# Kernel tuning notes

Measured on AMD Instinct MI355X. Metric: run time of the kernel, lower is better.

## Reference

```python
import jax, jax.numpy as jnp
import numpy as np

NUM_EMBEDDINGS = 1024
EMBEDDING_DIM = 64
COMMITMENT_COST = 0.25
EPS_NORM = 1e-12  # torch F.normalize eps


def _l2_normalize(x):
    n = jnp.linalg.norm(x, axis=-1, keepdims=True)
    return x / jnp.maximum(n, EPS_NORM)


def setup_inputs() -> dict:
    key = jax.random.key(0)
    k1, k2 = jax.random.split(key)
    inputs = jax.random.normal(k1, (16, 4096, EMBEDDING_DIM), dtype=jnp.float32)
    weight = jax.random.normal(k2, (NUM_EMBEDDINGS, EMBEDDING_DIM), dtype=jnp.float32) * 0.02
    return {"inputs": inputs, "weight": weight}


def reference(inputs, weight):
    input_shape = inputs.shape
    x = _l2_normalize(inputs)                      # [B,S,D]
    flat = x.reshape(-1, EMBEDDING_DIM)            # [N,D]
    w = _l2_normalize(weight)                      # [K,D]

    distances = (jnp.sum(flat ** 2, axis=1, keepdims=True)
                 + jnp.sum(w ** 2, axis=1)
                 - 2.0 * flat @ w.T)               # [N,K]
    encoding_indices = jnp.argmin(distances, axis=1)  # [N]

    quantized = w[encoding_indices].reshape(input_shape)  # [B,S,D]

    e_latent_loss = jnp.mean((jax.lax.stop_gradient(quantized) - x) ** 2)
    q_latent_loss = jnp.mean((quantized - jax.lax.stop_gradient(x)) ** 2)
    loss = q_latent_loss + COMMITMENT_COST * e_latent_loss

    # straight-through estimator
    quantized_ste = x + jax.lax.stop_gradient(quantized - x)

    # perplexity (no-grad bookkeeping)
    n = encoding_indices.shape[0]
    counts = jnp.zeros((NUM_EMBEDDINGS,), jnp.float32).at[encoding_indices].add(1.0)
    avg_probs = counts / n
    perplexity = jnp.exp(-jnp.sum(avg_probs * jnp.log(avg_probs + 1e-10)))

    return loss, quantized_ste, perplexity, encoding_indices[:, None]
```

## Files before the change

### kernel.cpp

```cpp
#include <hip/hip_runtime.h>
#include <hip/hip_bf16.h>
#include <math.h>

#define NROWS   65536
#define DIM     64
#define KCODES  1024
#define NBLOCKS (NROWS / 128)

#define QGAP 1.25e-4f

typedef short short8 __attribute__((ext_vector_type(8)));
typedef float f32x4  __attribute__((ext_vector_type(4)));

#define OUT_Q_OFF    ((size_t)1)
#define OUT_PERP_OFF ((size_t)(1 + (size_t)NROWS * DIM))
#define OUT_IDX_OFF  ((size_t)(2 + (size_t)NROWS * DIM))

#define WS_COUNTS 0
#define WS_SSEC   4096
#define WS_DONE   4100
#define WS_WN     8192
#define WS_SK     (WS_WN + KCODES*DIM*4)
#define WS_WNH    (WS_SK + KCODES*4)
#define WS_WNL    (WS_WNH + KCODES*DIM*2)

__device__ __forceinline__ unsigned short bf16_rne(float f) {
  unsigned u = __float_as_uint(f);
  return (unsigned short)((u + 0x7FFFu + ((u >> 16) & 1u)) >> 16);
}
__device__ __forceinline__ float bf16f(unsigned short h) {
  return __uint_as_float(((unsigned)h) << 16);
}

__global__ void __launch_bounds__(64) normalize_w_kernel(
    const float* __restrict__ w, float* __restrict__ wn, float* __restrict__ sk,
    unsigned short* __restrict__ wnh, unsigned short* __restrict__ wnl,
    unsigned* __restrict__ counts, float* __restrict__ sse_accum,
    unsigned* __restrict__ done) {
  const int k = blockIdx.x;
  const int d = threadIdx.x;
  if (d == 0) {
    counts[k] = 0u;
    if (k == 0) { *sse_accum = 0.f; *done = 0u; }
  }
  float v = w[k * DIM + d];
  float ss = v * v;
  #pragma unroll
  for (int o = 32; o > 0; o >>= 1) ss += __shfl_xor(ss, o, 64);
  const float den = fmaxf(sqrtf(ss), 1e-12f);
  const float q = v / den;
  wn[k * DIM + d] = q;
  const unsigned short h = bf16_rne(q);
  wnh[k * DIM + d] = h;
  wnl[k * DIM + d] = bf16_rne(q - bf16f(h));
  float s2 = q * q;
  #pragma unroll
  for (int o = 32; o > 0; o >>= 1) s2 += __shfl_xor(s2, o, 64);
  if (d == 0) sk[k] = s2;
}

__global__ void __launch_bounds__(256) vq_mega_kernel(
    const float* __restrict__ x, const unsigned short* __restrict__ wnh,
    const unsigned short* __restrict__ wnl, const float* __restrict__ sk,
    const float* __restrict__ wn, float* __restrict__ out,
    unsigned* __restrict__ counts, float* __restrict__ sse_accum,
    unsigned* __restrict__ done) {
  __shared__ unsigned AB[9216];
  __shared__ float skb[2][64];
  __shared__ float c_arr[128];
  __shared__ float rowsse[128];
  __shared__ int   ib[128];
  __shared__ int   qlist[128];
  __shared__ int   qn_s;
  __shared__ int   islast;
  const int tid = threadIdx.x;
  const int lane = tid & 63, wave = tid >> 6;

  if (tid == 0) qn_s = 0;

  if (tid < 128) {
    const size_t row = (size_t)blockIdx.x * 128 + tid;
    const float4* xr = (const float4*)(x + row * DIM);
    float4 xv[16];
    float ss = 0.f;
    #pragma unroll
    for (int i = 0; i < 16; i++) {
      xv[i] = xr[i];
      ss += xv[i].x * xv[i].x + xv[i].y * xv[i].y + xv[i].z * xv[i].z + xv[i].w * xv[i].w;
    }
    const float inv = 1.0f / fmaxf(sqrtf(ss), 1e-12f);
    float c = 0.f;
    #pragma unroll
    for (int i = 0; i < 16; i++) {
      const float a0 = xv[i].x * inv, a1 = xv[i].y * inv;
      const float a2 = xv[i].z * inv, a3 = xv[i].w * inv;
      c += a0 * a0 + a1 * a1 + a2 * a2 + a3 * a3;
      const unsigned short h0 = bf16_rne(a0), h1 = bf16_rne(a1);
      const unsigned short h2 = bf16_rne(a2), h3 = bf16_rne(a3);
      const unsigned short l0 = bf16_rne(a0 - bf16f(h0)), l1 = bf16_rne(a1 - bf16f(h1));
      const unsigned short l2 = bf16_rne(a2 - bf16f(h2)), l3 = bf16_rne(a3 - bf16f(h3));
      AB[tid * 36 + 2 * i]            = (unsigned)h0 | ((unsigned)h1 << 16);
      AB[tid * 36 + 2 * i + 1]        = (unsigned)h2 | ((unsigned)h3 << 16);
      AB[4608 + tid * 36 + 2 * i]     = (unsigned)l0 | ((unsigned)l1 << 16);
      AB[4608 + tid * 36 + 2 * i + 1] = (unsigned)l2 | ((unsigned)l3 << 16);
    }
    c_arr[tid] = c;
  }
  __syncthreads();

  short8 ah[2][2], al[2][2];
  #pragma unroll
  for (int rt = 0; rt < 2; rt++)
    #pragma unroll
    for (int kk = 0; kk < 2; kk++) {
      const int r = wave * 32 + rt * 16 + (lane & 15);
      ah[rt][kk] = *(const short8*)&AB[r * 36 + kk * 16 + (lane >> 4) * 4];
      al[rt][kk] = *(const short8*)&AB[4608 + r * 36 + kk * 16 + (lane >> 4) * 4];
    }
  __syncthreads();

  float d1[8], d2[8];
  int   i1[8];
  #pragma unroll
  for (int s = 0; s < 8; s++) { d1[s] = INFINITY; d2[s] = INFINITY; i1[s] = 0x7FFFFFFF; }

  {
    const int code = tid >> 2, q = tid & 3;
    const float4* gh = (const float4*)(wnh + (size_t)code * DIM + q * 16);
    const float4* gl = (const float4*)(wnl + (size_t)code * DIM + q * 16);
    float4* dh = (float4*)&AB[code * 36 + q * 8];
    float4* dl = (float4*)&AB[2304 + code * 36 + q * 8];
    dh[0] = gh[0]; dh[1] = gh[1];
    dl[0] = gl[0]; dl[1] = gl[1];
    if (tid < 64) skb[0][tid] = sk[tid];
  }

  #pragma unroll 2
  for (int c = 0; c < 16; c++) {
    const int b = c & 1;
    __syncthreads();
    if (c < 15) {
      const int nb = b ^ 1;
      const int code = tid >> 2, q = tid & 3;
      const float4* gh = (const float4*)(wnh + (size_t)((c + 1) * 64 + code) * DIM + q * 16);
      const float4* gl = (const float4*)(wnl + (size_t)((c + 1) * 64 + code) * DIM + q * 16);
      float4* dh = (float4*)&AB[nb * 4608 + code * 36 + q * 8];
      float4* dl = (float4*)&AB[nb * 4608 + 2304 + code * 36 + q * 8];
      dh[0] = gh[0]; dh[1] = gh[1];
      dl[0] = gl[0]; dl[1] = gl[1];
      if (tid < 64) skb[nb][tid] = sk[(c + 1) * 64 + tid];
    }
    #pragma unroll
    for (int tt = 0; tt < 4; tt++) {
      const int cb = tt * 16 + (lane & 15);
      const float skv = skb[b][cb];
      const int codev = c * 64 + cb;
      const short8 bh0 = *(const short8*)&AB[b * 4608 + cb * 36 + 0 * 16 + (lane >> 4) * 4];
      const short8 bh1 = *(const short8*)&AB[b * 4608 + cb * 36 + 1 * 16 + (lane >> 4) * 4];
      const short8 bl0 = *(const short8*)&AB[b * 4608 + 2304 + cb * 36 + 0 * 16 + (lane >> 4) * 4];
      const short8 bl1 = *(const short8*)&AB[b * 4608 + 2304 + cb * 36 + 1 * 16 + (lane >> 4) * 4];
      #pragma unroll
      for (int rt = 0; rt < 2; rt++) {
        f32x4 acc = {0.f, 0.f, 0.f, 0.f};
        acc = __builtin_amdgcn_mfma_f32_16x16x32_bf16(ah[rt][0], bh0, acc, 0, 0, 0);
        acc = __builtin_amdgcn_mfma_f32_16x16x32_bf16(ah[rt][1], bh1, acc, 0, 0, 0);
        acc = __builtin_amdgcn_mfma_f32_16x16x32_bf16(al[rt][0], bh0, acc, 0, 0, 0);
        acc = __builtin_amdgcn_mfma_f32_16x16x32_bf16(al[rt][1], bh1, acc, 0, 0, 0);
        acc = __builtin_amdgcn_mfma_f32_16x16x32_bf16(ah[rt][0], bl0, acc, 0, 0, 0);
        acc = __builtin_amdgcn_mfma_f32_16x16x32_bf16(ah[rt][1], bl1, acc, 0, 0, 0);
        #pragma unroll
        for (int i = 0; i < 4; i++) {
          const float dist = fmaf(-2.0f, acc[i], skv);
          const int s = rt * 4 + i;
          d2[s] = __builtin_amdgcn_fmed3f(d1[s], d2[s], dist);
          const bool take = dist < d1[s];
          d1[s] = take ? dist : d1[s];
          i1[s] = take ? codev : i1[s];
        }
      }
    }
  }

  #pragma unroll
  for (int s = 0; s < 8; s++) {
    float a1 = d1[s], a2 = d2[s];
    int   ai = i1[s];
    #pragma unroll
    for (int m = 1; m < 16; m <<= 1) {
      const float p1 = __shfl_xor(a1, m, 64);
      const float p2 = __shfl_xor(a2, m, 64);
      const int   pi = __shfl_xor(ai, m, 64);
      const float mx = fmaxf(a1, p1);
      a2 = fminf(fminf(a2, p2), mx);
      const bool take = (p1 < a1) || (p1 == a1 && pi < ai);
      a1 = take ? p1 : a1;
      ai = take ? pi : ai;
    }
    if ((lane & 15) == 0) {
      const int row_local = wave * 32 + (s >> 2) * 16 + (lane >> 4) * 4 + (s & 3);
      ib[row_local] = ai;
      rowsse[row_local] = a1 + c_arr[row_local];
      if (a2 - a1 < QGAP) qlist[atomicAdd(&qn_s, 1)] = row_local;
    }
  }
  __syncthreads();

  const int qn = qn_s;
  for (int qi = wave; qi < qn; qi += 4) {
    const int rl = qlist[qi];
    const size_t row = (size_t)blockIdx.x * 128 + rl;
    const float4* xr = (const float4*)(x + row * DIM);
    float4 xv[16];
    float ss = 0.f;
    #pragma unroll
    for (int i = 0; i < 16; i++) {
      xv[i] = xr[i];
      ss += xv[i].x * xv[i].x + xv[i].y * xv[i].y + xv[i].z * xv[i].z + xv[i].w * xv[i].w;
    }
    const float den = fmaxf(sqrtf(ss), 1e-12f);
    #pragma unroll
    for (int i = 0; i < 16; i++) { xv[i].x /= den; xv[i].y /= den; xv[i].z /= den; xv[i].w /= den; }
    float cc = 0.f;
    #pragma unroll
    for (int i = 0; i < 16; i++)
      cc += xv[i].x * xv[i].x + xv[i].y * xv[i].y + xv[i].z * xv[i].z + xv[i].w * xv[i].w;

    float best = INFINITY;
    int bidx = 0x7FFFFFFF;
    for (int j = 0; j < 16; j++) {
      const int k = j * 64 + lane;
      const float4* wr = (const float4*)(wn + (size_t)k * DIM);
      float e0 = 0.f, e1 = 0.f, e2 = 0.f, e3 = 0.f;
      #pragma unroll
      for (int i = 0; i < 16; i++) {
        const float4 wv = wr[i];
        e0 = fmaf(xv[i].x, wv.x, e0);
        e1 = fmaf(xv[i].y, wv.y, e1);
        e2 = fmaf(xv[i].z, wv.z, e2);
        e3 = fmaf(xv[i].w, wv.w, e3);
      }
      const float dot = (e0 + e1) + (e2 + e3);
      const float dist = (cc + sk[k]) - 2.0f * dot;
      if (dist < best) { best = dist; bidx = k; }
    }
    #pragma unroll
    for (int m = 1; m < 64; m <<= 1) {
      const float pb = __shfl_xor(best, m, 64);
      const int pi = __shfl_xor(bidx, m, 64);
      if (pb < best || (pb == best && pi < bidx)) { best = pb; bidx = pi; }
    }
    if (lane == 0) { ib[rl] = bidx; rowsse[rl] = best; }
  }
  __syncthreads();

  if (tid < 128) {
    const size_t row = (size_t)blockIdx.x * 128 + tid;
    const int idx = ib[tid];
    out[OUT_IDX_OFF + row] = (float)idx;
    atomicAdd(&counts[idx], 1u);
  }

  const size_t obase = OUT_Q_OFF + (size_t)blockIdx.x * (128 * DIM);
  #pragma unroll 4
  for (int j = 0; j < 32; j++) {
    const int e = j * 256 + tid;
    out[obase + e] = wn[(size_t)ib[e >> 6] * DIM + (e & 63)];
  }

  __syncthreads();
  for (int s = 64; s > 0; s >>= 1) {
    if (tid < s && tid + s < 128) rowsse[tid] += rowsse[tid + s];
    __syncthreads();
  }
  if (tid == 0) atomicAdd(sse_accum, rowsse[0]);

  if (tid == 0) {
    __threadfence();
    islast = (atomicAdd(done, 1u) == NBLOCKS - 1) ? 1 : 0;
  }
  __syncthreads();
  if (islast) {
    __threadfence();
    float h = 0.f;
    #pragma unroll
    for (int i = 0; i < 4; i++) {
      const float cv = (float)counts[tid * 4 + i];
      const float avg = cv * (1.0f / (float)NROWS);
      h += avg * logf(avg + 1e-10f);
    }
    #pragma unroll
    for (int o = 32; o > 0; o >>= 1) h += __shfl_xor(h, o, 64);
    __shared__ float hred[4];
    if (lane == 0) hred[wave] = h;
    __syncthreads();
    if (tid == 0) {
      const float H = -(hred[0] + hred[1] + hred[2] + hred[3]);
      const float mse = *sse_accum * (1.0f / (float)((size_t)NROWS * DIM));
      out[0] = mse + 0.25f * mse;
      out[OUT_PERP_OFF] = expf(H);
    }
  }
}

extern "C" void kernel_launch(void* const* d_in, const int* in_sizes, int n_in,
                              void* d_out, int out_size, void* d_ws, size_t ws_size,
                              hipStream_t stream) {
  const float* x = (const float*)d_in[0];
  const float* w = (const float*)d_in[1];
  float* out = (float*)d_out;

  char* ws = (char*)d_ws;
  unsigned* counts    = (unsigned*)(ws + WS_COUNTS);
  float* sse_accum    = (float*)(ws + WS_SSEC);
  unsigned* done      = (unsigned*)(ws + WS_DONE);
  float* wn           = (float*)(ws + WS_WN);
  float* sk           = (float*)(ws + WS_SK);
  unsigned short* wnh = (unsigned short*)(ws + WS_WNH);
  unsigned short* wnl = (unsigned short*)(ws + WS_WNL);

  normalize_w_kernel<<<KCODES, 64, 0, stream>>>(w, wn, sk, wnh, wnl,
                                                counts, sse_accum, done);
  vq_mega_kernel<<<NBLOCKS, 256, 0, stream>>>(
      x, wnh, wnl, sk, wn, out, counts, sse_accum, done);
}
```

Baseline: 144.8 us.

## Halve rows per block and track top-3 to cheapen near-tie rechecks

Rows per block drop from 128 to 64, which doubles the grid, and each wave now handles one 16-row tile instead of two. Input normalisation is split across four threads per row, with shuffle reductions. The argmin now tracks the best three distances and the top two indices. Rows whose top-2 gap is small but whose third candidate is clear get a cheap exact fp32 recheck of only two codes, one thread per row. Only rows with a three-way near tie fall back to the full 1024-code scan. The aim is better occupancy and less fallback work, at the cost of restaging the codebook twice as often (more L2 traffic) and extra comparison logic per distance.

```diff
diff --git a/kernel.cpp b/kernel.cpp
--- a/kernel.cpp
+++ b/kernel.cpp
@@ -5,7 +5,8 @@
 #define NROWS   65536
 #define DIM     64
 #define KCODES  1024
-#define NBLOCKS (NROWS / 128)
+#define RPB     64
+#define NBLOCKS (NROWS / RPB)
 
 #define QGAP 1.25e-4f
 
@@ -67,31 +68,35 @@
     unsigned* __restrict__ done) {
   __shared__ unsigned AB[9216];
   __shared__ float skb[2][64];
-  __shared__ float c_arr[128];
-  __shared__ float rowsse[128];
-  __shared__ int   ib[128];
-  __shared__ int   qlist[128];
-  __shared__ int   qn_s;
+  __shared__ float c_arr[RPB];
+  __shared__ float rowsse[RPB];
+  __shared__ int   ib[RPB];
+  __shared__ int   qlist[RPB];
+  __shared__ int   flist[RPB];
+  __shared__ int   qn_s, fn_s;
   __shared__ int   islast;
   const int tid = threadIdx.x;
   const int lane = tid & 63, wave = tid >> 6;
 
-  if (tid == 0) qn_s = 0;
-
-  if (tid < 128) {
-    const size_t row = (size_t)blockIdx.x * 128 + tid;
-    const float4* xr = (const float4*)(x + row * DIM);
-    float4 xv[16];
+  if (tid == 0) { qn_s = 0; fn_s = 0; }
+
+  {
+    const int row_l = tid >> 2;
+    const int qr = tid & 3;
+    const size_t row = (size_t)blockIdx.x * RPB + row_l;
+    const float4* xr = (const float4*)(x + row * DIM) + qr * 4;
+    float4 xv[4];
     float ss = 0.f;
     #pragma unroll
-    for (int i = 0; i < 16; i++) {
+    for (int i = 0; i < 4; i++) {
       xv[i] = xr[i];
       ss += xv[i].x * xv[i].x + xv[i].y * xv[i].y + xv[i].z * xv[i].z + xv[i].w * xv[i].w;
     }
+    ss += __shfl_xor(ss, 1, 64); ss += __shfl_xor(ss, 2, 64);
     const float inv = 1.0f / fmaxf(sqrtf(ss), 1e-12f);
     float c = 0.f;
     #pragma unroll
-    for (int i = 0; i < 16; i++) {
+    for (int i = 0; i < 4; i++) {
       const float a0 = xv[i].x * inv, a1 = xv[i].y * inv;
       const float a2 = xv[i].z * inv, a3 = xv[i].w * inv;
       c += a0 * a0 + a1 * a1 + a2 * a2 + a3 * a3;
@@ -99,30 +104,32 @@
       const unsigned short h2 = bf16_rne(a2), h3 = bf16_rne(a3);
       const unsigned short l0 = bf16_rne(a0 - bf16f(h0)), l1 = bf16_rne(a1 - bf16f(h1));
       const unsigned short l2 = bf16_rne(a2 - bf16f(h2)), l3 = bf16_rne(a3 - bf16f(h3));
-      AB[tid * 36 + 2 * i]            = (unsigned)h0 | ((unsigned)h1 << 16);
-      AB[tid * 36 + 2 * i + 1]        = (unsigned)h2 | ((unsigned)h3 << 16);
-      AB[4608 + tid * 36 + 2 * i]     = (unsigned)l0 | ((unsigned)l1 << 16);
-      AB[4608 + tid * 36 + 2 * i + 1] = (unsigned)l2 | ((unsigned)l3 << 16);
-    }
-    c_arr[tid] = c;
-  }
-  __syncthreads();
-
-  short8 ah[2][2], al[2][2];
-  #pragma unroll
-  for (int rt = 0; rt < 2; rt++)
-    #pragma unroll
-    for (int kk = 0; kk < 2; kk++) {
-      const int r = wave * 32 + rt * 16 + (lane & 15);
-      ah[rt][kk] = *(const short8*)&AB[r * 36 + kk * 16 + (lane >> 4) * 4];
-      al[rt][kk] = *(const short8*)&AB[4608 + r * 36 + kk * 16 + (lane >> 4) * 4];
-    }
-  __syncthreads();
-
-  float d1[8], d2[8];
-  int   i1[8];
-  #pragma unroll
-  for (int s = 0; s < 8; s++) { d1[s] = INFINITY; d2[s] = INFINITY; i1[s] = 0x7FFFFFFF; }
+      AB[row_l * 36 + qr * 8 + 2 * i]            = (unsigned)h0 | ((unsigned)h1 << 16);
+      AB[row_l * 36 + qr * 8 + 2 * i + 1]        = (unsigned)h2 | ((unsigned)h3 << 16);
+      AB[2304 + row_l * 36 + qr * 8 + 2 * i]     = (unsigned)l0 | ((unsigned)l1 << 16);
+      AB[2304 + row_l * 36 + qr * 8 + 2 * i + 1] = (unsigned)l2 | ((unsigned)l3 << 16);
+    }
+    c += __shfl_xor(c, 1, 64); c += __shfl_xor(c, 2, 64);
+    if (qr == 0) c_arr[row_l] = c;
+  }
+  __syncthreads();
+
+  short8 ah[2], al[2];
+  #pragma unroll
+  for (int kk = 0; kk < 2; kk++) {
+    const int r = wave * 16 + (lane & 15);
+    ah[kk] = *(const short8*)&AB[r * 36 + kk * 16 + (lane >> 4) * 4];
+    al[kk] = *(const short8*)&AB[2304 + r * 36 + kk * 16 + (lane >> 4) * 4];
+  }
+  __syncthreads();
+
+  float d1[4], d2[4], d3[4];
+  int   i1[4], i2[4];
+  #pragma unroll
+  for (int s = 0; s < 4; s++) {
+    d1[s] = INFINITY; d2[s] = INFINITY; d3[s] = INFINITY;
+    i1[s] = 0x7FFFFFFF; i2[s] = 0x7FFFFFFF;
+  }
 
   {
     const int code = tid >> 2, q = tid & 3;
@@ -159,56 +166,107 @@
       const short8 bh1 = *(const short8*)&AB[b * 4608 + cb * 36 + 1 * 16 + (lane >> 4) * 4];
       const short8 bl0 = *(const short8*)&AB[b * 4608 + 2304 + cb * 36 + 0 * 16 + (lane >> 4) * 4];
       const short8 bl1 = *(const short8*)&AB[b * 4608 + 2304 + cb * 36 + 1 * 16 + (lane >> 4) * 4];
+      f32x4 acc = {0.f, 0.f, 0.f, 0.f};
+      acc = __builtin_amdgcn_mfma_f32_16x16x32_bf16(ah[0], bh0, acc, 0, 0, 0);
+      acc = __builtin_amdgcn_mfma_f32_16x16x32_bf16(ah[1], bh1, acc, 0, 0, 0);
+      acc = __builtin_amdgcn_mfma_f32_16x16x32_bf16(al[0], bh0, acc, 0, 0, 0);
+      acc = __builtin_amdgcn_mfma_f32_16x16x32_bf16(al[1], bh1, acc, 0, 0, 0);
+      acc = __builtin_amdgcn_mfma_f32_16x16x32_bf16(ah[0], bl0, acc, 0, 0, 0);
+      acc = __builtin_amdgcn_mfma_f32_16x16x32_bf16(ah[1], bl1, acc, 0, 0, 0);
       #pragma unroll
-      for (int rt = 0; rt < 2; rt++) {
-        f32x4 acc = {0.f, 0.f, 0.f, 0.f};
-        acc = __builtin_amdgcn_mfma_f32_16x16x32_bf16(ah[rt][0], bh0, acc, 0, 0, 0);
-        acc = __builtin_amdgcn_mfma_f32_16x16x32_bf16(ah[rt][1], bh1, acc, 0, 0, 0);
-        acc = __builtin_amdgcn_mfma_f32_16x16x32_bf16(al[rt][0], bh0, acc, 0, 0, 0);
-        acc = __builtin_amdgcn_mfma_f32_16x16x32_bf16(al[rt][1], bh1, acc, 0, 0, 0);
-        acc = __builtin_amdgcn_mfma_f32_16x16x32_bf16(ah[rt][0], bl0, acc, 0, 0, 0);
-        acc = __builtin_amdgcn_mfma_f32_16x16x32_bf16(ah[rt][1], bl1, acc, 0, 0, 0);
-        #pragma unroll
-        for (int i = 0; i < 4; i++) {
-          const float dist = fmaf(-2.0f, acc[i], skv);
-          const int s = rt * 4 + i;
-          d2[s] = __builtin_amdgcn_fmed3f(d1[s], d2[s], dist);
-          const bool take = dist < d1[s];
-          d1[s] = take ? dist : d1[s];
-          i1[s] = take ? codev : i1[s];
-        }
+      for (int i = 0; i < 4; i++) {
+        const float dist = fmaf(-2.0f, acc[i], skv);
+        const int s = i;
+        d3[s] = __builtin_amdgcn_fmed3f(d2[s], d3[s], fmaxf(d1[s], dist));
+        const bool lt2 = dist < d2[s];
+        i2[s] = lt2 ? codev : i2[s];
+        d2[s] = __builtin_amdgcn_fmed3f(d1[s], d2[s], dist);
+        const bool lt1 = dist < d1[s];
+        i2[s] = lt1 ? i1[s] : i2[s];
+        i1[s] = lt1 ? codev : i1[s];
+        d1[s] = lt1 ? dist : d1[s];
       }
     }
   }
 
   #pragma unroll
-  for (int s = 0; s < 8; s++) {
-    float a1 = d1[s], a2 = d2[s];
-    int   ai = i1[s];
+  for (int s = 0; s < 4; s++) {
+    float a1 = d1[s], a2 = d2[s], a3 = d3[s];
+    int   ai = i1[s], ai2 = i2[s];
     #pragma unroll
     for (int m = 1; m < 16; m <<= 1) {
       const float p1 = __shfl_xor(a1, m, 64);
       const float p2 = __shfl_xor(a2, m, 64);
+      const float p3 = __shfl_xor(a3, m, 64);
       const int   pi = __shfl_xor(ai, m, 64);
-      const float mx = fmaxf(a1, p1);
-      a2 = fminf(fminf(a2, p2), mx);
+      const int   pi2 = __shfl_xor(ai2, m, 64);
       const bool take = (p1 < a1) || (p1 == a1 && pi < ai);
-      a1 = take ? p1 : a1;
-      ai = take ? pi : ai;
+      const float lo1 = take ? p1 : a1, lo2 = take ? p2 : a2, lo3 = take ? p3 : a3;
+      const float hi1 = take ? a1 : p1, hi2 = take ? a2 : p2;
+      const int   loi = take ? pi : ai, loi2 = take ? pi2 : ai2;
+      const int   hii = take ? ai : pi;
+      const bool c2 = hi1 < lo2;
+      a1 = lo1; ai = loi;
+      a2 = c2 ? hi1 : lo2; ai2 = c2 ? hii : loi2;
+      a3 = c2 ? fminf(lo2, hi2) : fminf(lo3, hi1);
     }
     if ((lane & 15) == 0) {
-      const int row_local = wave * 32 + (s >> 2) * 16 + (lane >> 4) * 4 + (s & 3);
+      const int row_local = wave * 16 + (lane >> 4) * 4 + s;
       ib[row_local] = ai;
       rowsse[row_local] = a1 + c_arr[row_local];
-      if (a2 - a1 < QGAP) qlist[atomicAdd(&qn_s, 1)] = row_local;
-    }
-  }
-  __syncthreads();
-
-  const int qn = qn_s;
-  for (int qi = wave; qi < qn; qi += 4) {
-    const int rl = qlist[qi];
-    const size_t row = (size_t)blockIdx.x * 128 + rl;
+      if (a3 - a1 < QGAP) {
+        flist[atomicAdd(&fn_s, 1)] = row_local;
+      } else if (a2 - a1 < QGAP) {
+        qlist[atomicAdd(&qn_s, 1)] = row_local | (ai << 6) | (ai2 << 16);
+      }
+    }
+  }
+  __syncthreads();
+
+  const int qn = qn_s, fn = fn_s;
+  if (tid < qn) {
+    const int packed = qlist[tid];
+    const int rl = packed & 63;
+    const int c1 = (packed >> 6) & 1023, c2i = (packed >> 16) & 1023;
+    const size_t row = (size_t)blockIdx.x * RPB + rl;
+    const float4* xr = (const float4*)(x + row * DIM);
+    float4 xv[16];
+    float ss = 0.f;
+    #pragma unroll
+    for (int i = 0; i < 16; i++) {
+      xv[i] = xr[i];
+      ss += xv[i].x * xv[i].x + xv[i].y * xv[i].y + xv[i].z * xv[i].z + xv[i].w * xv[i].w;
+    }
+    const float den = fmaxf(sqrtf(ss), 1e-12f);
+    #pragma unroll
+    for (int i = 0; i < 16; i++) { xv[i].x /= den; xv[i].y /= den; xv[i].z /= den; xv[i].w /= den; }
+    float cc = 0.f;
+    #pragma unroll
+    for (int i = 0; i < 16; i++)
+      cc += xv[i].x * xv[i].x + xv[i].y * xv[i].y + xv[i].z * xv[i].z + xv[i].w * xv[i].w;
+    float dd[2]; const int cand[2] = {c1, c2i};
+    #pragma unroll
+    for (int t = 0; t < 2; t++) {
+      const float4* wr = (const float4*)(wn + (size_t)cand[t] * DIM);
+      float e0 = 0.f, e1 = 0.f, e2 = 0.f, e3 = 0.f;
+      #pragma unroll
+      for (int i = 0; i < 16; i++) {
+        const float4 wv = wr[i];
+        e0 = fmaf(xv[i].x, wv.x, e0);
+        e1 = fmaf(xv[i].y, wv.y, e1);
+        e2 = fmaf(xv[i].z, wv.z, e2);
+        e3 = fmaf(xv[i].w, wv.w, e3);
+      }
+      dd[t] = (cc + sk[cand[t]]) - 2.0f * ((e0 + e1) + (e2 + e3));
+    }
+    const bool tb = (dd[1] < dd[0]) || (dd[1] == dd[0] && c2i < c1);
+    ib[rl] = tb ? c2i : c1;
+    rowsse[rl] = tb ? dd[1] : dd[0];
+  }
+
+  for (int qi = wave; qi < fn; qi += 4) {
+    const int rl = flist[qi];
+    const size_t row = (size_t)blockIdx.x * RPB + rl;
     const float4* xr = (const float4*)(x + row * DIM);
     float4 xv[16];
     float ss = 0.f;
@@ -253,23 +311,23 @@
   }
   __syncthreads();
 
-  if (tid < 128) {
-    const size_t row = (size_t)blockIdx.x * 128 + tid;
+  if (tid < RPB) {
+    const size_t row = (size_t)blockIdx.x * RPB + tid;
     const int idx = ib[tid];
     out[OUT_IDX_OFF + row] = (float)idx;
     atomicAdd(&counts[idx], 1u);
   }
 
-  const size_t obase = OUT_Q_OFF + (size_t)blockIdx.x * (128 * DIM);
+  const size_t obase = OUT_Q_OFF + (size_t)blockIdx.x * (RPB * DIM);
   #pragma unroll 4
-  for (int j = 0; j < 32; j++) {
+  for (int j = 0; j < 16; j++) {
     const int e = j * 256 + tid;
     out[obase + e] = wn[(size_t)ib[e >> 6] * DIM + (e & 63)];
   }
 
   __syncthreads();
-  for (int s = 64; s > 0; s >>= 1) {
-    if (tid < s && tid + s < 128) rowsse[tid] += rowsse[tid + s];
+  for (int s = 32; s > 0; s >>= 1) {
+    if (tid < s) rowsse[tid] += rowsse[tid + s];
     __syncthreads();
   }
   if (tid == 0) atomicAdd(sse_accum, rowsse[0]);
```

New measurement: 157.0 us. 1.08x slower.
